# Kernel tuning notes

Measured on AMD Instinct MI355X. Metric: run time of the kernel, lower is better.

Reference implementation:

```python
import jax, jax.numpy as jnp
import numpy as np

C = 256          # C_in == C_out
G = C // 4       # groups = C_in/4 -> 4 channels per group
K = 3
STRIDE = 1
PAD = 2
DIL = 2
EPS = 1e-5

@jax.custom_vjp
def binarize(x):
    # 1-bit sign binarization with straight-through estimator (STE)
    return jnp.sign(x)

def _bin_fwd(x):
    return jnp.sign(x), x

def _bin_bwd(x, g):
    # STE with hardtanh clip: pass grad where |x| <= 1
    return (g * (jnp.abs(x) <= 1.0).astype(g.dtype),)

binarize.defvjp(_bin_fwd, _bin_bwd)

def setup_inputs() -> dict:
    key = jax.random.key(0)
    k1, k2, k3, k4, k5, k6 = jax.random.split(key, 6)
    x = jax.random.normal(k1, (64, C, 32, 32), jnp.float32)
    # grouped conv weight: [C_out, C_in/groups, K, K] = [256, 4, 3, 3]
    weight = jax.random.normal(k2, (C, C // G, K, K), jnp.float32) * 0.1
    gamma = 1.0 + 0.1 * jax.random.normal(k3, (C,), jnp.float32)
    beta = 0.1 * jax.random.normal(k4, (C,), jnp.float32)
    running_mean = 0.1 * jax.random.normal(k5, (C,), jnp.float32)
    running_var = jax.random.uniform(k6, (C,), jnp.float32, 0.5, 1.5)
    return {"x": x, "weight": weight, "gamma": gamma, "beta": beta,
            "running_mean": running_mean, "running_var": running_var}

def reference(x, weight, gamma, beta, running_mean, running_var):
    # BatchNorm2d (inference form with running stats)
    inv = gamma * jax.lax.rsqrt(running_var + EPS)            # [C]
    h = x * inv[None, :, None, None] + (beta - running_mean * inv)[None, :, None, None]
    # binarize activations and weights (1w1a)
    a = binarize(h)
    w = binarize(weight)
    # grouped dilated conv, stride 1, pad 2, dilation 2 -> same HxW
    out = jax.lax.conv_general_dilated(
        a, w,
        window_strides=(STRIDE, STRIDE),
        padding=[(PAD, PAD), (PAD, PAD)],
        rhs_dilation=(DIL, DIL),
        dimension_numbers=("NCHW", "OIHW", "NCHW"),
        feature_group_count=G)
    # channel shuffle: [N,C,H,W] -> [N,g,C/g,H,W] -> [N,C/g,g,H,W] -> [N,C,H,W]
    N, Cc, H, W = out.shape
    out = out.reshape(N, G, Cc // G, H, W).transpose(0, 2, 1, 3, 4).reshape(N, Cc, H, W)
    # identity shortcut (stride == 1)
    return out + x
```

## Files before the change

### kernel.cpp

```cpp
#include <hip/hip_runtime.h>

#ifndef __has_builtin
#define __has_builtin(x) 0
#endif

#if __has_builtin(__builtin_amdgcn_sdot4)
#define DOT4(a, b, c) __builtin_amdgcn_sdot4((a), (b), (c), false)
#else
__device__ __forceinline__ int dot4_sw(int a, int b, int c) {
#pragma unroll
    for (int k = 0; k < 4; ++k)
        c += (int)(signed char)((a >> (8 * k)) & 0xff) *
             (int)(signed char)((b >> (8 * k)) & 0xff);
    return c;
}
#define DOT4(a, b, c) dot4_sw((a), (b), (c))
#endif

#if __has_builtin(__builtin_amdgcn_sched_barrier)
#define SCHED_FENCE() __builtin_amdgcn_sched_barrier(0)
#else
#define SCHED_FENCE() asm volatile("" ::: "memory")
#endif

typedef float vfloat4 __attribute__((ext_vector_type(4)));

constexpr int CH   = 256;
constexpr int NPIX = 1024;
constexpr float BN_EPS = 1e-5f;

__global__ __launch_bounds__(256, 4)
void bconv(const float* __restrict__ x,
           const float* __restrict__ wgt,
           const float* __restrict__ gamma,
           const float* __restrict__ beta,
           const float* __restrict__ rmean,
           const float* __restrict__ rvar,
           float* __restrict__ out) {
    const int tid = threadIdx.x;
    const int bid = blockIdx.x;
    const int swz = (bid & 7) * 256 + (bid >> 3);
    const int n0  = (swz >> 6) * 2;
    const int g   = swz & 63;

    const int pix0 = tid * 4;
    const int row  = pix0 >> 5;
    const int col0 = pix0 & 31;
    const float* xnA = x + n0 * CH * NPIX;
    const float* xnB = xnA + CH * NPIX;
    float* onA = out + n0 * CH * NPIX;
    float* onB = onA + CH * NPIX;

    vfloat4 xvA[3][4];
#pragma unroll
    for (int kh = 0; kh < 3; ++kh) {
        const int rsc = min(max(row + 2 * kh - 2, 0), 31);
        const float* rp = xnA + g * 4 * NPIX + rsc * 32 + col0;
#pragma unroll
        for (int ci = 0; ci < 4; ++ci)
            xvA[kh][ci] = *(const vfloat4*)(rp + ci * NPIX);
    }
    vfloat4 scA[4];
#pragma unroll
    for (int c2 = 0; c2 < 4; ++c2)
        scA[c2] = *(const vfloat4*)(xnA + (c2 * 64 + g) * NPIX + pix0);
    SCHED_FENCE();

    const int* wb = (const int*)(wgt + g * 144);
    int wq[4][9];
#pragma unroll
    for (int c2 = 0; c2 < 4; ++c2)
#pragma unroll
        for (int t = 0; t < 9; ++t) {
            int pk = 0;
#pragma unroll
            for (int ci = 0; ci < 4; ++ci) {
                const int b = wb[c2 * 36 + ci * 9 + t];
                const int s = ((b & 0x7fffffff) == 0) ? 0 : ((b < 0) ? -1 : 1);
                pk |= (s & 0xff) << (8 * ci);
            }
            wq[c2][t] = pk;
        }

    float inv[4], bias[4];
#pragma unroll
    for (int ci = 0; ci < 4; ++ci) {
        const int c = g * 4 + ci;
        float r  = __fdiv_rn(1.0f, __fsqrt_rn(__fadd_rn(rvar[c], BN_EPS)));
        inv[ci]  = __fmul_rn(gamma[c], r);
        bias[ci] = __fsub_rn(beta[c], __fmul_rn(rmean[c], inv[ci]));
    }

    auto pack = [&](const vfloat4 xv[3][4], int pkc[3][4]) {
#pragma unroll
        for (int kh = 0; kh < 3; ++kh) {
            const bool ok = (unsigned)(row + 2 * kh - 2) < 32u;
#pragma unroll
            for (int p = 0; p < 4; ++p) {
                int v = 0;
#pragma unroll
                for (int ci = 0; ci < 4; ++ci) {
                    float h = __fadd_rn(__fmul_rn(xv[kh][ci][p], inv[ci]), bias[ci]);
                    int s = (h > 0.f) ? 1 : ((h < 0.f) ? -1 : 0);
                    v |= (s & 0xff) << (8 * ci);
                }
                pkc[kh][p] = ok ? v : 0;
            }
        }
    };

    const bool le = (col0 == 0), re = (col0 == 28);
    auto compute_store = [&](const int pkc[3][4], const vfloat4 sc[4], float* on) {
        int a[3][8];
#pragma unroll
        for (int kh = 0; kh < 3; ++kh) {
            int l2 = __shfl_up(pkc[kh][2], 1);
            int l3 = __shfl_up(pkc[kh][3], 1);
            int r0 = __shfl_down(pkc[kh][0], 1);
            int r1 = __shfl_down(pkc[kh][1], 1);
            a[kh][0] = le ? 0 : l2;
            a[kh][1] = le ? 0 : l3;
            a[kh][2] = pkc[kh][0]; a[kh][3] = pkc[kh][1];
            a[kh][4] = pkc[kh][2]; a[kh][5] = pkc[kh][3];
            a[kh][6] = re ? 0 : r0;
            a[kh][7] = re ? 0 : r1;
        }
#pragma unroll
        for (int c2 = 0; c2 < 4; ++c2) {
            vfloat4 o;
#pragma unroll
            for (int p = 0; p < 4; ++p) {
                int acc = 0;
#pragma unroll
                for (int kh = 0; kh < 3; ++kh)
#pragma unroll
                    for (int kw = 0; kw < 3; ++kw)
                        acc = DOT4(a[kh][p + 2 * kw], wq[c2][kh * 3 + kw], acc);
                o[p] = __fadd_rn((float)acc, sc[c2][p]);
            }
            __builtin_nontemporal_store(o, (vfloat4*)(on + (c2 * 64 + g) * NPIX + pix0));
        }
    };

    int pkcA[3][4];
    pack(xvA, pkcA);

    vfloat4 xvB[3][4];
#pragma unroll
    for (int kh = 0; kh < 3; ++kh) {
        const int rsc = min(max(row + 2 * kh - 2, 0), 31);
        const float* rp = xnB + g * 4 * NPIX + rsc * 32 + col0;
#pragma unroll
        for (int ci = 0; ci < 4; ++ci)
            xvB[kh][ci] = *(const vfloat4*)(rp + ci * NPIX);
    }
    SCHED_FENCE();

    compute_store(pkcA, scA, onA);

    vfloat4 scB[4];
#pragma unroll
    for (int c2 = 0; c2 < 4; ++c2)
        scB[c2] = *(const vfloat4*)(xnB + (c2 * 64 + g) * NPIX + pix0);
    SCHED_FENCE();

    int pkcB[3][4];
    pack(xvB, pkcB);
    compute_store(pkcB, scB, onB);
}

extern "C" void kernel_launch(void* const* d_in, const int* in_sizes, int n_in,
                              void* d_out, int out_size, void* d_ws, size_t ws_size,
                              hipStream_t stream) {
    const float* x     = (const float*)d_in[0];
    const float* wgt   = (const float*)d_in[1];
    const float* gamma = (const float*)d_in[2];
    const float* beta  = (const float*)d_in[3];
    const float* rmean = (const float*)d_in[4];
    const float* rvar  = (const float*)d_in[5];
    float* out = (float*)d_out;

    const int N = in_sizes[0] / (CH * NPIX);
    bconv<<<(N / 2) * 64, 256, 0, stream>>>(x, wgt, gamma, beta, rmean, rvar, out);
}
```

Before: 30.52 us.

## Split work into single-wavefront blocks of eight rows per image and group

Each block now holds one 64-lane wavefront that covers an 8-row slice of one image for one channel group, instead of 256 threads covering two images in sequence. The grid grows eightfold, the launch bound drops to 64, and the manual two-image software pipeline is removed. The aim is finer scheduling granularity, fewer registers per thread and higher occupancy. In exchange, each block recomputes the weight packing and BN constants and reloads the halo rows above and below its slice, and there is more block launch overhead.

```diff
diff --git a/kernel.cpp b/kernel.cpp
--- a/kernel.cpp
+++ b/kernel.cpp
@@ -29,7 +29,7 @@
 constexpr int NPIX = 1024;
 constexpr float BN_EPS = 1e-5f;
 
-__global__ __launch_bounds__(256, 4)
+__global__ __launch_bounds__(64)
 void bconv(const float* __restrict__ x,
            const float* __restrict__ wgt,
            const float* __restrict__ gamma,
@@ -37,33 +37,32 @@
            const float* __restrict__ rmean,
            const float* __restrict__ rvar,
            float* __restrict__ out) {
-    const int tid = threadIdx.x;
+    const int lane = threadIdx.x;
     const int bid = blockIdx.x;
-    const int swz = (bid & 7) * 256 + (bid >> 3);
-    const int n0  = (swz >> 6) * 2;
-    const int g   = swz & 63;
+    const int swz = (bid & 7) * 2048 + (bid >> 3);
+    const int oct = swz & 3;
+    const int g   = (swz >> 2) & 63;
+    const int n   = swz >> 8;
 
-    const int pix0 = tid * 4;
-    const int row  = pix0 >> 5;
-    const int col0 = pix0 & 31;
-    const float* xnA = x + n0 * CH * NPIX;
-    const float* xnB = xnA + CH * NPIX;
-    float* onA = out + n0 * CH * NPIX;
-    float* onB = onA + CH * NPIX;
+    const int row  = oct * 8 + (lane >> 3);
+    const int col0 = (lane & 7) * 4;
+    const int pix0 = row * 32 + col0;
+    const float* xn = x + n * CH * NPIX;
+    float* on = out + n * CH * NPIX;
 
-    vfloat4 xvA[3][4];
+    vfloat4 xv[3][4];
 #pragma unroll
     for (int kh = 0; kh < 3; ++kh) {
         const int rsc = min(max(row + 2 * kh - 2, 0), 31);
-        const float* rp = xnA + g * 4 * NPIX + rsc * 32 + col0;
+        const float* rp = xn + g * 4 * NPIX + rsc * 32 + col0;
 #pragma unroll
         for (int ci = 0; ci < 4; ++ci)
-            xvA[kh][ci] = *(const vfloat4*)(rp + ci * NPIX);
+            xv[kh][ci] = *(const vfloat4*)(rp + ci * NPIX);
     }
-    vfloat4 scA[4];
+    vfloat4 sc[4];
 #pragma unroll
     for (int c2 = 0; c2 < 4; ++c2)
-        scA[c2] = *(const vfloat4*)(xnA + (c2 * 64 + g) * NPIX + pix0);
+        sc[c2] = *(const vfloat4*)(xn + (c2 * 64 + g) * NPIX + pix0);
     SCHED_FENCE();
 
     const int* wb = (const int*)(wgt + g * 144);
@@ -91,82 +90,54 @@
         bias[ci] = __fsub_rn(beta[c], __fmul_rn(rmean[c], inv[ci]));
     }
 
-    auto pack = [&](const vfloat4 xv[3][4], int pkc[3][4]) {
+    int pkc[3][4];
 #pragma unroll
-        for (int kh = 0; kh < 3; ++kh) {
-            const bool ok = (unsigned)(row + 2 * kh - 2) < 32u;
+    for (int kh = 0; kh < 3; ++kh) {
+        const bool ok = (unsigned)(row + 2 * kh - 2) < 32u;
 #pragma unroll
-            for (int p = 0; p < 4; ++p) {
-                int v = 0;
+        for (int p = 0; p < 4; ++p) {
+            int v = 0;
 #pragma unroll
-                for (int ci = 0; ci < 4; ++ci) {
-                    float h = __fadd_rn(__fmul_rn(xv[kh][ci][p], inv[ci]), bias[ci]);
-                    int s = (h > 0.f) ? 1 : ((h < 0.f) ? -1 : 0);
-                    v |= (s & 0xff) << (8 * ci);
-                }
-                pkc[kh][p] = ok ? v : 0;
+            for (int ci = 0; ci < 4; ++ci) {
+                float h = __fadd_rn(__fmul_rn(xv[kh][ci][p], inv[ci]), bias[ci]);
+                int s = (h > 0.f) ? 1 : ((h < 0.f) ? -1 : 0);
+                v |= (s & 0xff) << (8 * ci);
             }
+            pkc[kh][p] = ok ? v : 0;
         }
-    };
+    }
 
     const bool le = (col0 == 0), re = (col0 == 28);
-    auto compute_store = [&](const int pkc[3][4], const vfloat4 sc[4], float* on) {
-        int a[3][8];
-#pragma unroll
-        for (int kh = 0; kh < 3; ++kh) {
-            int l2 = __shfl_up(pkc[kh][2], 1);
-            int l3 = __shfl_up(pkc[kh][3], 1);
-            int r0 = __shfl_down(pkc[kh][0], 1);
-            int r1 = __shfl_down(pkc[kh][1], 1);
-            a[kh][0] = le ? 0 : l2;
-            a[kh][1] = le ? 0 : l3;
-            a[kh][2] = pkc[kh][0]; a[kh][3] = pkc[kh][1];
-            a[kh][4] = pkc[kh][2]; a[kh][5] = pkc[kh][3];
-            a[kh][6] = re ? 0 : r0;
-            a[kh][7] = re ? 0 : r1;
-        }
-#pragma unroll
-        for (int c2 = 0; c2 < 4; ++c2) {
-            vfloat4 o;
-#pragma unroll
-            for (int p = 0; p < 4; ++p) {
-                int acc = 0;
-#pragma unroll
-                for (int kh = 0; kh < 3; ++kh)
-#pragma unroll
-                    for (int kw = 0; kw < 3; ++kw)
-                        acc = DOT4(a[kh][p + 2 * kw], wq[c2][kh * 3 + kw], acc);
-                o[p] = __fadd_rn((float)acc, sc[c2][p]);
-            }
-            __builtin_nontemporal_store(o, (vfloat4*)(on + (c2 * 64 + g) * NPIX + pix0));
-        }
-    };
-
-    int pkcA[3][4];
-    pack(xvA, pkcA);
-
-    vfloat4 xvB[3][4];
+    int a[3][8];
 #pragma unroll
     for (int kh = 0; kh < 3; ++kh) {
-        const int rsc = min(max(row + 2 * kh - 2, 0), 31);
-        const float* rp = xnB + g * 4 * NPIX + rsc * 32 + col0;
+        int l2 = __shfl_up(pkc[kh][2], 1);
+        int l3 = __shfl_up(pkc[kh][3], 1);
+        int r0 = __shfl_down(pkc[kh][0], 1);
+        int r1 = __shfl_down(pkc[kh][1], 1);
+        a[kh][0] = le ? 0 : l2;
+        a[kh][1] = le ? 0 : l3;
+        a[kh][2] = pkc[kh][0]; a[kh][3] = pkc[kh][1];
+        a[kh][4] = pkc[kh][2]; a[kh][5] = pkc[kh][3];
+        a[kh][6] = re ? 0 : r0;
+        a[kh][7] = re ? 0 : r1;
+    }
+
 #pragma unroll
-        for (int ci = 0; ci < 4; ++ci)
-            xvB[kh][ci] = *(const vfloat4*)(rp + ci * NPIX);
+    for (int c2 = 0; c2 < 4; ++c2) {
+        vfloat4 o;
+#pragma unroll
+        for (int p = 0; p < 4; ++p) {
+            int acc = 0;
+#pragma unroll
+            for (int kh = 0; kh < 3; ++kh)
+#pragma unroll
+                for (int kw = 0; kw < 3; ++kw)
+                    acc = DOT4(a[kh][p + 2 * kw], wq[c2][kh * 3 + kw], acc);
+            o[p] = __fadd_rn((float)acc, sc[c2][p]);
+        }
+        __builtin_nontemporal_store(o, (vfloat4*)(on + (c2 * 64 + g) * NPIX + pix0));
     }
-    SCHED_FENCE();
-
-    compute_store(pkcA, scA, onA);
-
-    vfloat4 scB[4];
-#pragma unroll
-    for (int c2 = 0; c2 < 4; ++c2)
-        scB[c2] = *(const vfloat4*)(xnB + (c2 * 64 + g) * NPIX + pix0);
-    SCHED_FENCE();
-
-    int pkcB[3][4];
-    pack(xvB, pkcB);
-    compute_store(pkcB, scB, onB);
 }
 
 extern "C" void kernel_launch(void* const* d_in, const int* in_sizes, int n_in,
@@ -181,5 +152,5 @@
     float* out = (float*)d_out;
 
     const int N = in_sizes[0] / (CH * NPIX);
-    bconv<<<(N / 2) * 64, 256, 0, stream>>>(x, wgt, gamma, beta, rmean, rvar, out);
+    bconv<<<N * 64 * 4, 64, 0, stream>>>(x, wgt, gamma, beta, rmean, rvar, out);
 }
```

After: 35.53 us. +16.4%, slower.
